# Kernel optimization log

Measured on AMD Instinct MI355X. Metric: run time of the kernel, lower is better.

Reference implementation:

```python
import jax, jax.numpy as jnp
import numpy as np

B, SX, SY, D = 32, 2048, 2048, 160

def setup_inputs() -> dict:
    key = jax.random.key(0)
    ks = jax.random.split(key, 5)
    s = 1.0 / np.sqrt(D)
    return {
        "x": jax.random.normal(ks[0], (B, SX, D), dtype=jnp.float32),
        "y": jax.random.normal(ks[1], (B, SY, D), dtype=jnp.float32),
        "Wq": jax.random.normal(ks[2], (D, D), dtype=jnp.float32) * s,
        "bq": jnp.zeros((D,), dtype=jnp.float32),
        "Wk": jax.random.normal(ks[3], (D, D), dtype=jnp.float32) * s,
        "bk": jnp.zeros((D,), dtype=jnp.float32),
        "Wv": jax.random.normal(ks[4], (D, D), dtype=jnp.float32) * s,
        "bv": jnp.zeros((D,), dtype=jnp.float32),
    }

def reference(x, y, Wq, bq, Wk, bk, Wv, bv):
    # torch nn.Linear: out = in @ W.T + b, W is [out_dim, in_dim]
    q = jnp.einsum('bxd,ed->bxe', x, Wq) + bq          # [B,SX,D]
    k = jnp.einsum('byd,ed->bye', y, Wk) + bk          # [B,SY,D]
    v = jnp.einsum('byd,ed->bye', y, Wv) + bv          # [B,SY,D]
    scores = jnp.einsum('bxd,byd->bxy', q, k)          # [B,SX,SY] (no scaling in source)
    attn = jax.nn.softmax(scores, axis=-1)
    out = jnp.einsum('bxy,byd->bxd', attn, v)          # dropout is identity at eval
    return out + x                                     # residual
```

## Files before the change

kernel.cpp:

```cpp
#include <hip/hip_runtime.h>

#define LOG2E 1.44269504088896340736f

typedef _Float16 f16;
typedef __attribute__((ext_vector_type(4))) _Float16 f16x4;
typedef __attribute__((ext_vector_type(8))) _Float16 f16x8;
typedef __attribute__((ext_vector_type(4))) float f32x4;
typedef __attribute__((ext_vector_type(8))) unsigned short us8;

#define BB 32
#define SSX 2048
#define SSY 2048
#define DD 160
#define M_TOTAL (BB*SSX)

#define PRS 168
#define VTRS 136
#define RS 168
#define P_RS 72

__device__ __forceinline__ f32x4 mfma16(f16x8 a, f16x8 b, f32x4 c) {
  return __builtin_amdgcn_mfma_f32_16x16x32_f16(a, b, c, 0, 0, 0);
}

__global__ __launch_bounds__(256, 2) void proj_kernel(
    const float* __restrict__ x, const float* __restrict__ y,
    const float* __restrict__ Wq, const float* __restrict__ bq,
    const float* __restrict__ Wk, const float* __restrict__ bk,
    const float* __restrict__ Wv, const float* __restrict__ bv,
    f16* __restrict__ Qw, f16* __restrict__ Kw, f16* __restrict__ Vtw)
{
  __shared__ __align__(16) f16 buf[160*PRS];
  const int t = threadIdx.x;
  const int wave = t >> 6;
  const int lane = t & 63;
  const int quad = lane >> 4;
  const int l16  = lane & 15;
  const int bid  = blockIdx.x;
  const int kind = bid % 3;
  const int tile = bid / 3;
  const int row0 = tile * 128;
  const float* src  = (kind == 0) ? x  : y;
  const float* W    = (kind == 0) ? Wq : (kind == 1 ? Wk : Wv);
  const float* bias = (kind == 0) ? bq : (kind == 1 ? bk : bv);

  for (int i = 0; i < 20; ++i) {
    int idx = t + i*256;
    int r = idx / 40, c4 = idx % 40;
    float4 v = *(const float4*)&src[(size_t)(row0 + r)*DD + c4*4];
    f16x4 h = { (f16)v.x, (f16)v.y, (f16)v.z, (f16)v.w };
    *(f16x4*)&buf[r*PRS + c4*4] = h;
  }
  __syncthreads();
  f16x8 afr0[5], afr1[5];
  #pragma unroll
  for (int ks = 0; ks < 5; ++ks) {
    afr0[ks] = *(const f16x8*)&buf[(wave*32 + l16)*PRS + ks*32 + quad*8];
    afr1[ks] = *(const f16x8*)&buf[(wave*32 + 16 + l16)*PRS + ks*32 + quad*8];
  }
  __syncthreads();

  for (int i = 0; i < 25; ++i) {
    int idx = t + i*256;
    int r = idx / 40, c4 = idx % 40;
    float4 v = *(const float4*)&W[r*160 + c4*4];
    f16x4 h = { (f16)v.x, (f16)v.y, (f16)v.z, (f16)v.w };
    *(f16x4*)&buf[r*PRS + c4*4] = h;
  }
  __syncthreads();

  f32x4 acc0[10], acc1[10];
  #pragma unroll
  for (int nt = 0; nt < 10; ++nt) {
    float bs = bias[nt*16 + l16];
    acc0[nt] = (f32x4){bs,bs,bs,bs};
    acc1[nt] = (f32x4){bs,bs,bs,bs};
    #pragma unroll
    for (int ks = 0; ks < 5; ++ks) {
      f16x8 bfr = *(const f16x8*)&buf[(nt*16 + l16)*PRS + ks*32 + quad*8];
      acc0[nt] = mfma16(afr0[ks], bfr, acc0[nt]);
      acc1[nt] = mfma16(afr1[ks], bfr, acc1[nt]);
    }
  }
  __syncthreads();

  if (kind < 2) {
    f16* dst = (kind == 0) ? Qw : Kw;
    #pragma unroll
    for (int nt = 0; nt < 10; ++nt)
      #pragma unroll
      for (int r = 0; r < 4; ++r) {
        buf[(wave*32 + quad*4 + r)*PRS + nt*16 + l16]      = (f16)acc0[nt][r];
        buf[(wave*32 + 16 + quad*4 + r)*PRS + nt*16 + l16] = (f16)acc1[nt][r];
      }
    __syncthreads();
    for (int i = 0; i < 10; ++i) {
      int idx = t + i*256;
      int r = idx / 20, g = idx % 20;
      *(us8*)&dst[(size_t)(row0 + r)*DD + g*8] = *(const us8*)&buf[r*PRS + g*8];
    }
  } else {
    #pragma unroll
    for (int nt = 0; nt < 10; ++nt)
      #pragma unroll
      for (int r = 0; r < 4; ++r) {
        buf[(nt*16 + l16)*VTRS + wave*32 + quad*4 + r]      = (f16)acc0[nt][r];
        buf[(nt*16 + l16)*VTRS + wave*32 + 16 + quad*4 + r] = (f16)acc1[nt][r];
      }
    __syncthreads();
    const int b  = row0 / SSY;
    const int y0 = row0 % SSY;
    for (int i = 0; i < 10; ++i) {
      int idx = t + i*256;
      int d = idx / 16, yg = idx % 16;
      *(us8*)&Vtw[((size_t)b*DD + d)*SSY + y0 + yg*8] = *(const us8*)&buf[d*VTRS + yg*8];
    }
  }
}


#define LOAD_CHUNK(yb) { \
  const f16* ksrc = Kw + ((size_t)b*SSY + (yb))*DD; \
  const f16* vsrc = Vtw + (size_t)b*DD*SSY + (yb); \
  _Pragma("unroll") \
  for (int i = 0; i < 5; ++i) { \
    int idx = t + i*256; int r = idx/20, c = idx%20; \
    kreg[i] = *(const us8*)&ksrc[(size_t)r*DD + c*8]; \
  } \
  _Pragma("unroll") \
  for (int i = 0; i < 5; ++i) { \
    int idx = t + i*256; int d = idx>>3, g = idx&7; \
    vreg[i] = *(const us8*)&vsrc[(size_t)d*SSY + g*8]; \
  } \
}

#define STORE_CHUNK() { \
  _Pragma("unroll") \
  for (int i = 0; i < 5; ++i) { \
    int idx = t + i*256; int r = idx/20, c = idx%20; \
    *(us8*)&K_lds[r*RS + c*8] = kreg[i]; \
  } \
  _Pragma("unroll") \
  for (int i = 0; i < 5; ++i) { \
    int idx = t + i*256; int d = idx>>3, g = idx&7; \
    *(us8*)&Vt_lds[d*64 + ((g ^ (d & 7)) << 3)] = vreg[i]; \
  } \
}

__global__ __launch_bounds__(256, 2) void flash_kernel(
    const f16* __restrict__ Qw, const f16* __restrict__ Kw, const f16* __restrict__ Vtw,
    const float* __restrict__ x, float* __restrict__ out)
{
  __shared__ __align__(16) f16 K_lds[64*RS];
  __shared__ __align__(16) f16 Vt_lds[176*64];
  __shared__ __align__(16) f16 P_lds[4*32*P_RS];
  const int t = threadIdx.x;
  const int wave = t >> 6;
  const int lane = t & 63;
  const int quad = lane >> 4;
  const int l16  = lane & 15;
  const int bid  = blockIdx.x;
  const int b    = bid >> 4;
  const int x0   = (bid & 15) * 128;

  for (int idx = t; idx < 1024; idx += 256) {
    int d = idx >> 6, yy = idx & 63;
    Vt_lds[(160 + d)*64 + yy] = (d == 0) ? (f16)1.0f : (f16)0.0f;
  }

  f16x8 qfr0[5], qfr1[5];
  #pragma unroll
  for (int h = 0; h < 2; ++h) {
    if (h) __syncthreads();
    const f16* qsrc = Qw + ((size_t)b*SSX + x0 + h*64)*DD;
    for (int i = 0; i < 5; ++i) {
      int idx = t + i*256;
      int r = idx / 20, c = idx % 20;
      *(us8*)&K_lds[r*RS + c*8] = *(const us8*)&qsrc[(size_t)r*DD + c*8];
    }
    __syncthreads();
    if ((wave >> 1) == h) {
      const int base = (wave & 1)*32;
      #pragma unroll
      for (int ks = 0; ks < 5; ++ks) {
        qfr0[ks] = *(const f16x8*)&K_lds[(base + l16)*RS + ks*32 + quad*8];
        qfr1[ks] = *(const f16x8*)&K_lds[(base + 16 + l16)*RS + ks*32 + quad*8];
      }
    }
  }

  f32x4 acc0[11], acc1[11];
  #pragma unroll
  for (int i = 0; i < 11; ++i) { acc0[i] = (f32x4){0.f,0.f,0.f,0.f}; acc1[i] = (f32x4){0.f,0.f,0.f,0.f}; }
  float m0[4], m1[4];
  #pragma unroll
  for (int r = 0; r < 4; ++r) { m0[r] = -1e30f; m1[r] = -1e30f; }

  f16* Pw = &P_lds[wave*32*P_RS];
  us8 kreg[5], vreg[5];

  LOAD_CHUNK(0);
  for (int yc = 0; yc < SSY/64; ++yc) {
    __syncthreads();
    STORE_CHUNK();
    __syncthreads();
    if (yc < SSY/64 - 1) LOAD_CHUNK((yc+1)*64);

    f32x4 S0[4], S1[4];
    #pragma unroll
    for (int nt = 0; nt < 4; ++nt) { S0[nt] = (f32x4){0.f,0.f,0.f,0.f}; S1[nt] = (f32x4){0.f,0.f,0.f,0.f}; }
    #pragma unroll
    for (int nt = 0; nt < 4; ++nt)
      #pragma unroll
      for (int ks = 0; ks < 5; ++ks) {
        f16x8 kfr = *(const f16x8*)&K_lds[(nt*16 + l16)*RS + ks*32 + quad*8];
        S0[nt] = mfma16(qfr0[ks], kfr, S0[nt]);
        S1[nt] = mfma16(qfr1[ks], kfr, S1[nt]);
      }

    float n0[4], n1[4];
    bool changed = false;
    #pragma unroll
    for (int r = 0; r < 4; ++r) {
      float a = fmaxf(fmaxf(S0[0][r], S0[1][r]), fmaxf(S0[2][r], S0[3][r]));
      #pragma unroll
      for (int off = 1; off < 16; off <<= 1) a = fmaxf(a, __shfl_xor(a, off));
      n0[r] = fmaxf(m0[r], a);
      changed = changed || (n0[r] > m0[r]);
      float c = fmaxf(fmaxf(S1[0][r], S1[1][r]), fmaxf(S1[2][r], S1[3][r]));
      #pragma unroll
      for (int off = 1; off < 16; off <<= 1) c = fmaxf(c, __shfl_xor(c, off));
      n1[r] = fmaxf(m1[r], c);
      changed = changed || (n1[r] > m1[r]);
    }
    if (__any(changed)) {
      f32x4 av0, av1;
      #pragma unroll
      for (int r = 0; r < 4; ++r) {
        av0[r] = exp2f((m0[r] - n0[r])*LOG2E); m0[r] = n0[r];
        av1[r] = exp2f((m1[r] - n1[r])*LOG2E); m1[r] = n1[r];
      }
      #pragma unroll
      for (int i = 0; i < 11; ++i) { acc0[i] *= av0; acc1[i] *= av1; }
    }

    #pragma unroll
    for (int r = 0; r < 4; ++r)
      #pragma unroll
      for (int nt = 0; nt < 4; ++nt) {
        Pw[(quad*4 + r)*P_RS + nt*16 + l16]      = (f16)exp2f((S0[nt][r] - m0[r])*LOG2E);
        Pw[(16 + quad*4 + r)*P_RS + nt*16 + l16] = (f16)exp2f((S1[nt][r] - m1[r])*LOG2E);
      }

    #pragma unroll
    for (int k2 = 0; k2 < 2; ++k2) {
      f16x8 p0 = *(const f16x8*)&Pw[l16*P_RS + k2*32 + quad*8];
      f16x8 p1 = *(const f16x8*)&Pw[(16 + l16)*P_RS + k2*32 + quad*8];
      #pragma unroll
      for (int dt = 0; dt < 11; ++dt) {
        f16x8 vfr = *(const f16x8*)&Vt_lds[(dt*16 + l16)*64 + (((k2*4 + quad) ^ (l16 & 7)) << 3)];
        acc0[dt] = mfma16(p0, vfr, acc0[dt]);
        acc1[dt] = mfma16(p1, vfr, acc1[dt]);
      }
    }
  }

  float rl0[4], rl1[4];
  #pragma unroll
  for (int r = 0; r < 4; ++r) {
    rl0[r] = 1.f / __shfl(acc0[10][r], lane & 48);
    rl1[r] = 1.f / __shfl(acc1[10][r], lane & 48);
  }
  const size_t base = ((size_t)b*SSX + x0 + wave*32)*DD;
  #pragma unroll
  for (int dt = 0; dt < 10; ++dt)
    #pragma unroll
    for (int r = 0; r < 4; ++r) {
      size_t o0 = base + (size_t)(quad*4 + r)*DD + dt*16 + l16;
      size_t o1 = base + (size_t)(16 + quad*4 + r)*DD + dt*16 + l16;
      out[o0] = acc0[dt][r]*rl0[r] + x[o0];
      out[o1] = acc1[dt][r]*rl1[r] + x[o1];
    }
}

extern "C" void kernel_launch(void* const* d_in, const int* in_sizes, int n_in,
                              void* d_out, int out_size, void* d_ws, size_t ws_size,
                              hipStream_t stream) {
  const float* x  = (const float*)d_in[0];
  const float* y  = (const float*)d_in[1];
  const float* Wq = (const float*)d_in[2];
  const float* bq = (const float*)d_in[3];
  const float* Wk = (const float*)d_in[4];
  const float* bk = (const float*)d_in[5];
  const float* Wv = (const float*)d_in[6];
  const float* bv = (const float*)d_in[7];

  f16* Qw  = (f16*)d_ws;
  f16* Kw  = Qw + (size_t)M_TOTAL*DD;
  f16* Vtw = Kw + (size_t)M_TOTAL*DD;

  proj_kernel<<<1536, 256, 0, stream>>>(x, y, Wq, bq, Wk, bk, Wv, bv, Qw, Kw, Vtw);
  flash_kernel<<<512, 256, 0, stream>>>(Qw, Kw, Vtw, x, (float*)d_out);
}
```

Measured before the change: 325.6 us.

## Alias P buffer onto K LDS, pre-convert weights, shrink projection tiles, DPP row max

A small kernel now converts the three weight matrices to fp16 once. The projection kernel reads those fp16 weights straight from global memory and uses 64-row tiles at higher occupancy, instead of staging fp32 weights through LDS in every block. The flash kernel drops its separate P buffer and reuses the K LDS region, which needs an extra barrier after the QK^T MFMAs. That LDS saving is meant to allow 3 blocks per CU. Row-max shuffles are replaced with DPP row_shr reductions. The extra barrier adds synchronization, and with 512 blocks there may be too few blocks to use the higher occupancy.

```diff
diff --git a/kernel.cpp b/kernel.cpp
--- a/kernel.cpp
+++ b/kernel.cpp
@@ -15,7 +15,7 @@
 #define M_TOTAL (BB*SSX)
 
 #define PRS 168
-#define VTRS 136
+#define V2RS 72
 #define RS 168
 #define P_RS 72
 
@@ -23,14 +23,34 @@
   return __builtin_amdgcn_mfma_f32_16x16x32_f16(a, b, c, 0, 0, 0);
 }
 
-__global__ __launch_bounds__(256, 2) void proj_kernel(
+__device__ __forceinline__ float rmax16(float x) {
+  x = fmaxf(x, __int_as_float(__builtin_amdgcn_update_dpp(0, __float_as_int(x), 0x121, 0xf, 0xf, true)));
+  x = fmaxf(x, __int_as_float(__builtin_amdgcn_update_dpp(0, __float_as_int(x), 0x122, 0xf, 0xf, true)));
+  x = fmaxf(x, __int_as_float(__builtin_amdgcn_update_dpp(0, __float_as_int(x), 0x124, 0xf, 0xf, true)));
+  x = fmaxf(x, __int_as_float(__builtin_amdgcn_update_dpp(0, __float_as_int(x), 0x128, 0xf, 0xf, true)));
+  return x;
+}
+
+__global__ __launch_bounds__(256) void wconv_kernel(
+    const float* __restrict__ Wq, const float* __restrict__ Wk, const float* __restrict__ Wv,
+    f16* __restrict__ Wf)
+{
+  const int bid = blockIdx.x;
+  const int kind = bid / 25;
+  const int j = (bid % 25)*1024 + threadIdx.x*4;
+  const float* W = (kind == 0) ? Wq : (kind == 1 ? Wk : Wv);
+  float4 v = *(const float4*)&W[j];
+  f16x4 h = { (f16)v.x, (f16)v.y, (f16)v.z, (f16)v.w };
+  *(f16x4*)&Wf[kind*25600 + j] = h;
+}
+
+__global__ __launch_bounds__(256, 4) void proj_kernel(
     const float* __restrict__ x, const float* __restrict__ y,
-    const float* __restrict__ Wq, const float* __restrict__ bq,
-    const float* __restrict__ Wk, const float* __restrict__ bk,
-    const float* __restrict__ Wv, const float* __restrict__ bv,
+    const f16* __restrict__ Wf16,
+    const float* __restrict__ bq, const float* __restrict__ bk, const float* __restrict__ bv,
     f16* __restrict__ Qw, f16* __restrict__ Kw, f16* __restrict__ Vtw)
 {
-  __shared__ __align__(16) f16 buf[160*PRS];
+  __shared__ __align__(16) f16 buf[160*V2RS];
   const int t = threadIdx.x;
   const int wave = t >> 6;
   const int lane = t & 63;
@@ -39,12 +59,12 @@
   const int bid  = blockIdx.x;
   const int kind = bid % 3;
   const int tile = bid / 3;
-  const int row0 = tile * 128;
+  const int row0 = tile * 64;
   const float* src  = (kind == 0) ? x  : y;
-  const float* W    = (kind == 0) ? Wq : (kind == 1 ? Wk : Wv);
+  const f16*   Wf   = Wf16 + kind*25600;
   const float* bias = (kind == 0) ? bq : (kind == 1 ? bk : bv);
 
-  for (int i = 0; i < 20; ++i) {
+  for (int i = 0; i < 10; ++i) {
     int idx = t + i*256;
     int r = idx / 40, c4 = idx % 40;
     float4 v = *(const float4*)&src[(size_t)(row0 + r)*DD + c4*4];
@@ -52,34 +72,20 @@
     *(f16x4*)&buf[r*PRS + c4*4] = h;
   }
   __syncthreads();
-  f16x8 afr0[5], afr1[5];
-  #pragma unroll
-  for (int ks = 0; ks < 5; ++ks) {
-    afr0[ks] = *(const f16x8*)&buf[(wave*32 + l16)*PRS + ks*32 + quad*8];
-    afr1[ks] = *(const f16x8*)&buf[(wave*32 + 16 + l16)*PRS + ks*32 + quad*8];
-  }
-  __syncthreads();
-
-  for (int i = 0; i < 25; ++i) {
-    int idx = t + i*256;
-    int r = idx / 40, c4 = idx % 40;
-    float4 v = *(const float4*)&W[r*160 + c4*4];
-    f16x4 h = { (f16)v.x, (f16)v.y, (f16)v.z, (f16)v.w };
-    *(f16x4*)&buf[r*PRS + c4*4] = h;
-  }
-  __syncthreads();
-
-  f32x4 acc0[10], acc1[10];
+  f16x8 afr[5];
+  #pragma unroll
+  for (int ks = 0; ks < 5; ++ks)
+    afr[ks] = *(const f16x8*)&buf[(wave*16 + l16)*PRS + ks*32 + quad*8];
+
+  f32x4 acc[10];
   #pragma unroll
   for (int nt = 0; nt < 10; ++nt) {
     float bs = bias[nt*16 + l16];
-    acc0[nt] = (f32x4){bs,bs,bs,bs};
-    acc1[nt] = (f32x4){bs,bs,bs,bs};
+    acc[nt] = (f32x4){bs,bs,bs,bs};
     #pragma unroll
     for (int ks = 0; ks < 5; ++ks) {
-      f16x8 bfr = *(const f16x8*)&buf[(nt*16 + l16)*PRS + ks*32 + quad*8];
-      acc0[nt] = mfma16(afr0[ks], bfr, acc0[nt]);
-      acc1[nt] = mfma16(afr1[ks], bfr, acc1[nt]);
+      f16x8 bfr = *(const f16x8*)&Wf[(nt*16 + l16)*160 + ks*32 + quad*8];
+      acc[nt] = mfma16(afr[ks], bfr, acc[nt]);
     }
   }
   __syncthreads();
@@ -89,12 +95,10 @@
     #pragma unroll
     for (int nt = 0; nt < 10; ++nt)
       #pragma unroll
-      for (int r = 0; r < 4; ++r) {
-        buf[(wave*32 + quad*4 + r)*PRS + nt*16 + l16]      = (f16)acc0[nt][r];
-        buf[(wave*32 + 16 + quad*4 + r)*PRS + nt*16 + l16] = (f16)acc1[nt][r];
-      }
-    __syncthreads();
-    for (int i = 0; i < 10; ++i) {
+      for (int r = 0; r < 4; ++r)
+        buf[(wave*16 + quad*4 + r)*PRS + nt*16 + l16] = (f16)acc[nt][r];
+    __syncthreads();
+    for (int i = 0; i < 5; ++i) {
       int idx = t + i*256;
       int r = idx / 20, g = idx % 20;
       *(us8*)&dst[(size_t)(row0 + r)*DD + g*8] = *(const us8*)&buf[r*PRS + g*8];
@@ -103,17 +107,15 @@
     #pragma unroll
     for (int nt = 0; nt < 10; ++nt)
       #pragma unroll
-      for (int r = 0; r < 4; ++r) {
-        buf[(nt*16 + l16)*VTRS + wave*32 + quad*4 + r]      = (f16)acc0[nt][r];
-        buf[(nt*16 + l16)*VTRS + wave*32 + 16 + quad*4 + r] = (f16)acc1[nt][r];
-      }
+      for (int r = 0; r < 4; ++r)
+        buf[(nt*16 + l16)*V2RS + wave*16 + quad*4 + r] = (f16)acc[nt][r];
     __syncthreads();
     const int b  = row0 / SSY;
     const int y0 = row0 % SSY;
-    for (int i = 0; i < 10; ++i) {
+    for (int i = 0; i < 5; ++i) {
       int idx = t + i*256;
-      int d = idx / 16, yg = idx % 16;
-      *(us8*)&Vtw[((size_t)b*DD + d)*SSY + y0 + yg*8] = *(const us8*)&buf[d*VTRS + yg*8];
+      int d = idx / 8, yg = idx % 8;
+      *(us8*)&Vtw[((size_t)b*DD + d)*SSY + y0 + yg*8] = *(const us8*)&buf[d*V2RS + yg*8];
     }
   }
 }
@@ -147,13 +149,12 @@
   } \
 }
 
-__global__ __launch_bounds__(256, 2) void flash_kernel(
+__global__ __launch_bounds__(256, 3) void flash_kernel(
     const f16* __restrict__ Qw, const f16* __restrict__ Kw, const f16* __restrict__ Vtw,
     const float* __restrict__ x, float* __restrict__ out)
 {
   __shared__ __align__(16) f16 K_lds[64*RS];
   __shared__ __align__(16) f16 Vt_lds[176*64];
-  __shared__ __align__(16) f16 P_lds[4*32*P_RS];
   const int t = threadIdx.x;
   const int wave = t >> 6;
   const int lane = t & 63;
@@ -196,7 +197,7 @@
   #pragma unroll
   for (int r = 0; r < 4; ++r) { m0[r] = -1e30f; m1[r] = -1e30f; }
 
-  f16* Pw = &P_lds[wave*32*P_RS];
+  f16* Pw = &K_lds[wave*32*P_RS];
   us8 kreg[5], vreg[5];
 
   LOAD_CHUNK(0);
@@ -217,20 +218,17 @@
         S0[nt] = mfma16(qfr0[ks], kfr, S0[nt]);
         S1[nt] = mfma16(qfr1[ks], kfr, S1[nt]);
       }
+    __syncthreads();
 
     float n0[4], n1[4];
     bool changed = false;
     #pragma unroll
     for (int r = 0; r < 4; ++r) {
       float a = fmaxf(fmaxf(S0[0][r], S0[1][r]), fmaxf(S0[2][r], S0[3][r]));
-      #pragma unroll
-      for (int off = 1; off < 16; off <<= 1) a = fmaxf(a, __shfl_xor(a, off));
-      n0[r] = fmaxf(m0[r], a);
+      n0[r] = fmaxf(m0[r], rmax16(a));
       changed = changed || (n0[r] > m0[r]);
       float c = fmaxf(fmaxf(S1[0][r], S1[1][r]), fmaxf(S1[2][r], S1[3][r]));
-      #pragma unroll
-      for (int off = 1; off < 16; off <<= 1) c = fmaxf(c, __shfl_xor(c, off));
-      n1[r] = fmaxf(m1[r], c);
+      n1[r] = fmaxf(m1[r], rmax16(c));
       changed = changed || (n1[r] > m1[r]);
     }
     if (__any(changed)) {
@@ -298,7 +296,9 @@
   f16* Qw  = (f16*)d_ws;
   f16* Kw  = Qw + (size_t)M_TOTAL*DD;
   f16* Vtw = Kw + (size_t)M_TOTAL*DD;
-
-  proj_kernel<<<1536, 256, 0, stream>>>(x, y, Wq, bq, Wk, bk, Wv, bv, Qw, Kw, Vtw);
+  f16* Wf  = Vtw + (size_t)M_TOTAL*DD;
+
+  wconv_kernel<<<75, 256, 0, stream>>>(Wq, Wk, Wv, Wf);
+  proj_kernel<<<3072, 256, 0, stream>>>(x, y, Wf, bq, bk, bv, Qw, Kw, Vtw);
   flash_kernel<<<512, 256, 0, stream>>>(Qw, Kw, Vtw, x, (float*)d_out);
 }
```

Result: slower. 783.3 us (+140.5%).
